# Optimization experiments

Hardware: AMD Instinct MI355X
Metric: run time of the kernel (lower is better)

Reference implementation:

```python
import jax, jax.numpy as jnp
import numpy as np

N = 100000   # nodes
E = 1600000  # directed edges
D_IN, D_HID, D_OUT, N_CLS = 128, 256, 128, 10
EPS = 1e-5


def gcn_conv(x, W, b, src, dst, n):
    # PyG GCNConv: h = XW, add self loops, sym-normalize, scatter-add to dst, + bias
    h = x @ W
    loop = jnp.arange(n)
    src_f = jnp.concatenate([src, loop])
    dst_f = jnp.concatenate([dst, loop])
    deg = jax.ops.segment_sum(jnp.ones(src_f.shape[0], h.dtype), dst_f, num_segments=n)
    dinv = jnp.where(deg > 0, jax.lax.rsqrt(deg), jnp.zeros_like(deg))
    norm = dinv[src_f] * dinv[dst_f]                    # [E+N]
    out = jax.ops.segment_sum(h[src_f] * norm[:, None], dst_f, num_segments=n)
    return out + b


def batchnorm(x, gamma, beta):
    # training-mode BatchNorm1d (batch statistics, biased variance)
    mu = x.mean(0)
    var = x.var(0)
    return gamma * (x - mu) * jax.lax.rsqrt(var + EPS) + beta


def setup_inputs() -> dict:
    key = jax.random.key(0)
    ks = jax.random.split(key, 12)
    x = jax.random.normal(ks[0], (N, D_IN), jnp.float32)
    edge_index = jax.random.randint(ks[1], (2, E), 0, N, dtype=jnp.int64)
    def lin(k, fi, fo):
        s = 1.0 / np.sqrt(fi)
        return jax.random.uniform(k, (fi, fo), jnp.float32, -s, s)
    return {
        "x": x, "edge_index": edge_index,
        "W1": lin(ks[2], D_IN, D_HID), "b1": jnp.zeros(D_HID, jnp.float32),
        "g1": jnp.ones(D_HID, jnp.float32), "beta1": jnp.zeros(D_HID, jnp.float32),
        "W2": lin(ks[3], D_HID, D_HID), "b2": jnp.zeros(D_HID, jnp.float32),
        "g2": jnp.ones(D_HID, jnp.float32), "beta2": jnp.zeros(D_HID, jnp.float32),
        "W3": lin(ks[4], D_HID, D_OUT), "b3": jnp.zeros(D_OUT, jnp.float32),
        "g3": jnp.ones(D_OUT, jnp.float32), "beta3": jnp.zeros(D_OUT, jnp.float32),
        "Wout": lin(ks[5], D_OUT, N_CLS), "bout": jnp.zeros(N_CLS, jnp.float32),
    }


def reference(x, edge_index, W1, b1, g1, beta1, W2, b2, g2, beta2,
              W3, b3, g3, beta3, Wout, bout):
    src, dst = edge_index[0], edge_index[1]
    h = jax.nn.relu(batchnorm(gcn_conv(x, W1, b1, src, dst, N), g1, beta1))
    h = jax.nn.relu(batchnorm(gcn_conv(h, W2, b2, src, dst, N), g2, beta2))
    h = jax.nn.relu(batchnorm(gcn_conv(h, W3, b3, src, dst, N), g3, beta3))
    return h @ Wout + bout
```

## Files before the change

kernel.cpp:

```cpp
#include <hip/hip_runtime.h>
#include <hip/hip_fp16.h>
#include <cstdint>
#include <cstddef>

#define EPS_BN 1e-5f
#define NSLICE 16

static inline int cdiv(int a, int b) { return (a + b - 1) / b; }

using half8   = __attribute__((ext_vector_type(8))) _Float16;
using floatx4 = __attribute__((ext_vector_type(4))) float;

__device__ __forceinline__ float atomAddF(float* p, float v) {
    return unsafeAtomicAdd(p, v);
}


__global__ __launch_bounds__(256) void k_hist(const int* __restrict__ dst, int E,
                                              int NBLK, int NBUCK, int* __restrict__ H) {
    __shared__ int h[256];
    int t = threadIdx.x;
    h[t] = 0;
    __syncthreads();
    int base = blockIdx.x * 4096;
#pragma unroll
    for (int j = 0; j < 16; ++j) {
        int e = base + j * 256 + t;
        if (e < E) atomicAdd(&h[dst[e] >> 9], 1);
    }
    __syncthreads();
    if (t < NBUCK) H[t * NBLK + blockIdx.x] = h[t];
}

__global__ __launch_bounds__(256) void k_scan_reduce(const int* __restrict__ in, int m,
                                                     int* __restrict__ bsum) {
    int base = blockIdx.x * 1024;
    int t = threadIdx.x;
    int s = 0;
#pragma unroll
    for (int i = 0; i < 4; ++i) {
        int idx = base + t * 4 + i;
        if (idx < m) s += in[idx];
    }
    __shared__ int sm[256];
    sm[t] = s;
    __syncthreads();
    for (int off = 128; off > 0; off >>= 1) {
        if (t < off) sm[t] += sm[t + off];
        __syncthreads();
    }
    if (t == 0) bsum[blockIdx.x] = sm[0];
}

__global__ void k_scan_bsum(int* __restrict__ bsum, int nb) {
    if (threadIdx.x == 0 && blockIdx.x == 0) {
        int acc = 0;
        for (int i = 0; i < nb; ++i) { int v = bsum[i]; bsum[i] = acc; acc += v; }
    }
}

__global__ __launch_bounds__(256) void k_scan_final(const int* __restrict__ in, int m,
                                                    const int* __restrict__ bsum,
                                                    int* __restrict__ outS) {
    int base = blockIdx.x * 1024;
    int t = threadIdx.x;
    int v[4];
    int s = 0;
#pragma unroll
    for (int i = 0; i < 4; ++i) {
        int idx = base + t * 4 + i;
        v[i] = (idx < m) ? in[idx] : 0;
        s += v[i];
    }
    __shared__ int sm[256];
    sm[t] = s;
    __syncthreads();
    for (int off = 1; off < 256; off <<= 1) {
        int x = (t >= off) ? sm[t - off] : 0;
        __syncthreads();
        sm[t] += x;
        __syncthreads();
    }
    int excl = sm[t] - s + bsum[blockIdx.x];
#pragma unroll
    for (int i = 0; i < 4; ++i) {
        int idx = base + t * 4 + i;
        if (idx < m) { outS[idx] = excl; excl += v[i]; }
    }
}

__global__ __launch_bounds__(256) void k_bucket(const int* __restrict__ src,
                                                const int* __restrict__ dst, int E,
                                                int NBLK, int NBUCK,
                                                const int* __restrict__ S,
                                                unsigned* __restrict__ pairs) {
    __shared__ int cur[256];
    int t = threadIdx.x;
    if (t < NBUCK) cur[t] = S[t * NBLK + blockIdx.x];
    __syncthreads();
    int base = blockIdx.x * 4096;
#pragma unroll
    for (int j = 0; j < 16; ++j) {
        int e = base + j * 256 + t;
        if (e < E) {
            unsigned s = (unsigned)src[e];
            unsigned d = (unsigned)dst[e];
            int p = atomicAdd(&cur[d >> 9], 1);
            pairs[p] = ((d & 511u) << 17) | s;
        }
    }
}

__global__ __launch_bounds__(256) void k_build(const unsigned* __restrict__ pairs,
                                               const int* __restrict__ S,
                                               int NBLK, int NBUCK, int n, int E,
                                               int* __restrict__ endoff,
                                               float* __restrict__ dinv,
                                               int* __restrict__ csr) {
    int b = blockIdx.x;
    int nbase = b << 9;
    int bstart = S[b * NBLK];
    int bend = (b == NBUCK - 1) ? E : S[(b + 1) * NBLK];
    int t = threadIdx.x;
    __shared__ int sdeg[512];
    __shared__ int scur[512];
    __shared__ int stmp[256];
    sdeg[t] = 0; sdeg[t + 256] = 0;
    __syncthreads();
    for (int e = bstart + t; e < bend; e += 256)
        atomicAdd(&sdeg[pairs[e] >> 17], 1);
    __syncthreads();
    int d0 = sdeg[2 * t], d1 = sdeg[2 * t + 1];
    int ps = d0 + d1;
    stmp[t] = ps;
    __syncthreads();
    for (int off = 1; off < 256; off <<= 1) {
        int x = (t >= off) ? stmp[t - off] : 0;
        __syncthreads();
        stmp[t] += x;
        __syncthreads();
    }
    int c0 = bstart + stmp[t] - ps;
    int c1 = c0 + d0;
    scur[2 * t] = c0;
    scur[2 * t + 1] = c1;
    int v0 = nbase + 2 * t, v1 = v0 + 1;
    if (v0 < n) { endoff[v0] = c1;      dinv[v0] = rsqrtf((float)(d0 + 1)); }
    if (v1 < n) { endoff[v1] = c1 + d1; dinv[v1] = rsqrtf((float)(d1 + 1)); }
    __syncthreads();
    for (int e = bstart + t; e < bend; e += 256) {
        unsigned p = pairs[e];
        int pos = atomicAdd(&scur[p >> 17], 1);
        csr[pos] = (int)(p & 0x1FFFFu);
    }
}

__global__ __launch_bounds__(256) void k_prep(const float* __restrict__ x,
                                              const float* __restrict__ dinv,
                                              const float* __restrict__ W1,
                                              const float* __restrict__ W2,
                                              const float* __restrict__ W3,
                                              __half* __restrict__ xh,
                                              __half* __restrict__ Wt1,
                                              __half* __restrict__ Wt2,
                                              __half* __restrict__ Wt3,
                                              float* __restrict__ stats, int n) {
    int idx = blockIdx.x * 256 + threadIdx.x;
    int nx = n * 16;
    if (idx < nx) {
        int row = idx >> 4;
        float dv = dinv[row];
        const float4* p = (const float4*)x + (size_t)idx * 2;
        float4 a = p[0], b = p[1];
        uint4 o; __half2* oh = (__half2*)&o;
        oh[0] = __floats2half2_rn(a.x * dv, a.y * dv);
        oh[1] = __floats2half2_rn(a.z * dv, a.w * dv);
        oh[2] = __floats2half2_rn(b.x * dv, b.y * dv);
        oh[3] = __floats2half2_rn(b.z * dv, b.w * dv);
        ((uint4*)xh)[idx] = o;
        return;
    }
    int r = idx - nx;
    if (r < 32768) {
        int k = r >> 8, c = r & 255;
        Wt1[c * 128 + k] = __float2half(W1[r]);
    } else if (r < 98304) {
        int r2 = r - 32768;
        int k = r2 >> 8, c = r2 & 255;
        Wt2[c * 256 + k] = __float2half(W2[r2]);
    } else if (r < 131072) {
        int r2 = r - 98304;
        int k = r2 >> 7, c = r2 & 127;
        Wt3[c * 256 + k] = __float2half(W3[r2]);
    } else if (r < 131072 + NSLICE * 256 * 6) {
        stats[r - 131072] = 0.f;
    }
}

__device__ __forceinline__ void acc8(float* acc, uint4 d) {
    const __half2* h = (const __half2*)&d;
#pragma unroll
    for (int j = 0; j < 4; ++j) {
        float2 f = __half22float2(h[j]);
        acc[2 * j] += f.x; acc[2 * j + 1] += f.y;
    }
}

template<int D, bool STATS>
__global__ __launch_bounds__(256, 8) void k_gather_h(const int* __restrict__ csr,
                                                     const int* __restrict__ endoff,
                                                     const __half* __restrict__ P,
                                                     const float* __restrict__ dinv,
                                                     __half* __restrict__ S, int n,
                                                     float* __restrict__ sums,
                                                     float* __restrict__ sqs) {
    constexpr int LPN = D / 8;
    constexpr int NPB = 256 / LPN;
    __shared__ float red[STATS ? 2048 : 1];
    int t = threadIdx.x;
    int lane = t % LPN;
    int sub = t / LPN;
    int v = blockIdx.x * NPB + sub;
    float ov[8];
#pragma unroll
    for (int j = 0; j < 8; ++j) ov[j] = 0.f;
    if (v < n) {
        int beg = (v == 0) ? 0 : endoff[v - 1];
        int end = endoff[v];
        float acc[8];
        {
            uint4 d = *((const uint4*)(P + (size_t)v * D) + lane);
            const __half2* h = (const __half2*)&d;
#pragma unroll
            for (int j = 0; j < 4; ++j) {
                float2 f = __half22float2(h[j]);
                acc[2 * j] = f.x; acc[2 * j + 1] = f.y;
            }
        }
        int i = beg;
        int rem = (end - beg) & 3;
        if (rem & 2) {
            uint4 d0 = *((const uint4*)(P + (size_t)csr[i] * D) + lane);
            uint4 d1 = *((const uint4*)(P + (size_t)csr[i + 1] * D) + lane);
            acc8(acc, d0); acc8(acc, d1);
            i += 2;
        }
        if (rem & 1) {
            uint4 d0 = *((const uint4*)(P + (size_t)csr[i] * D) + lane);
            acc8(acc, d0);
            i += 1;
        }
        if (i < end) {
            uint4 a[4];
#pragma unroll
            for (int u = 0; u < 4; ++u)
                a[u] = *((const uint4*)(P + (size_t)csr[i + u] * D) + lane);
            for (i += 4; i < end; i += 4) {
                uint4 b[4];
#pragma unroll
                for (int u = 0; u < 4; ++u)
                    b[u] = *((const uint4*)(P + (size_t)csr[i + u] * D) + lane);
#pragma unroll
                for (int u = 0; u < 4; ++u) acc8(acc, a[u]);
#pragma unroll
                for (int u = 0; u < 4; ++u) a[u] = b[u];
            }
#pragma unroll
            for (int u = 0; u < 4; ++u) acc8(acc, a[u]);
        }
        float dv = dinv[v];
        uint4 o; __half2* oh = (__half2*)&o;
#pragma unroll
        for (int j = 0; j < 4; ++j) {
            float a0 = acc[2 * j] * dv, a1 = acc[2 * j + 1] * dv;
            oh[j] = __floats2half2_rn(a0, a1);
            ov[2 * j] = a0; ov[2 * j + 1] = a1;
        }
        *((uint4*)(S + (size_t)v * D) + lane) = o;
    }
    if (STATS) {
        int slice = blockIdx.x & (NSLICE - 1);
#pragma unroll
        for (int j = 0; j < 8; ++j) red[t * 8 + j] = ov[j];
        __syncthreads();
        if (t < D) {
            int lc = t >> 3, j = t & 7;
            float ts = 0.f;
#pragma unroll
            for (int s = 0; s < NPB; ++s) ts += red[(s * LPN + lc) * 8 + j];
            atomAddF(&sums[slice * 256 + t], ts);
        }
        __syncthreads();
#pragma unroll
        for (int j = 0; j < 8; ++j) red[t * 8 + j] = ov[j] * ov[j];
        __syncthreads();
        if (t < D) {
            int lc = t >> 3, j = t & 7;
            float tq = 0.f;
#pragma unroll
            for (int s = 0; s < NPB; ++s) tq += red[(s * LPN + lc) * 8 + j];
            atomAddF(&sqs[slice * 256 + t], tq);
        }
    }
}

template<int K, int NC, bool SCALE, bool BNIN, bool STATS>
__global__ __launch_bounds__(256) void k_gemm_mfma(const __half* __restrict__ A,
                                                   const __half* __restrict__ Wt,
                                                   const float* __restrict__ dinv,
                                                   const float* __restrict__ isum,
                                                   const float* __restrict__ isq,
                                                   const float* __restrict__ g,
                                                   const float* __restrict__ beta,
                                                   float* __restrict__ osum,
                                                   float* __restrict__ osq,
                                                   __half* __restrict__ C, int n) {
    constexpr int LDA = 40;
    __shared__ _Float16 As[128 * LDA];
    __shared__ _Float16 Bs[128 * LDA];
    __shared__ float ssc[BNIN ? K : 1];
    __shared__ float ssh[BNIN ? K : 1];
    __shared__ float scs[STATS ? 128 : 1];
    __shared__ float scq[STATS ? 128 : 1];
    int tid = threadIdx.x;
    if (BNIN) {
        float nf = (float)n;
        for (int i = tid; i < K; i += 256) {
            float su = 0.f, sq = 0.f;
#pragma unroll
            for (int s = 0; s < NSLICE; ++s) {
                su += isum[s * 256 + i];
                sq += isq[s * 256 + i];
            }
            float mu = su / nf;
            float var = sq / nf - mu * mu;
            float sc = g[i] * rsqrtf(var + EPS_BN);
            ssc[i] = sc; ssh[i] = beta[i] - mu * sc;
        }
        __syncthreads();
    }
    int wave = tid >> 6, lane = tid & 63;
    int wr = wave >> 1, wc = wave & 1;
    int q = lane >> 4, l16 = lane & 15;
    int row0 = blockIdx.x * 128;
    int col0 = blockIdx.y * 128;
    floatx4 acc[4][4];
#pragma unroll
    for (int r = 0; r < 4; ++r)
#pragma unroll
        for (int c = 0; c < 4; ++c) acc[r][c] = (floatx4)0.0f;

    for (int k0 = 0; k0 < K; k0 += 32) {
#pragma unroll
        for (int i = 0; i < 2; ++i) {
            int s = tid + i * 256;
            int r = s >> 2, ks = s & 3;
            uint4 d = *(const uint4*)(A + (size_t)(row0 + r) * K + k0 + ks * 8);
            if (BNIN) {
                const __half2* h = (const __half2*)&d;
                uint4 o; __half2* oh = (__half2*)&o;
                int kb = k0 + ks * 8;
#pragma unroll
                for (int j = 0; j < 4; ++j) {
                    float2 f = __half22float2(h[j]);
                    float y0 = fmaxf(0.f, f.x * ssc[kb + 2 * j]     + ssh[kb + 2 * j]);
                    float y1 = fmaxf(0.f, f.y * ssc[kb + 2 * j + 1] + ssh[kb + 2 * j + 1]);
                    oh[j] = __floats2half2_rn(y0, y1);
                }
                d = o;
            }
            *(uint4*)&As[r * LDA + ks * 8] = d;
        }
#pragma unroll
        for (int i = 0; i < 2; ++i) {
            int s = tid + i * 256;
            int r = s >> 2, ks = s & 3;
            uint4 d = *(const uint4*)(Wt + (size_t)(col0 + r) * K + k0 + ks * 8);
            *(uint4*)&Bs[r * LDA + ks * 8] = d;
        }
        __syncthreads();
        half8 af[4], bf[4];
#pragma unroll
        for (int r = 0; r < 4; ++r)
            af[r] = *(const half8*)&As[(wr * 64 + r * 16 + l16) * LDA + q * 8];
#pragma unroll
        for (int c = 0; c < 4; ++c)
            bf[c] = *(const half8*)&Bs[(wc * 64 + c * 16 + l16) * LDA + q * 8];
#pragma unroll
        for (int r = 0; r < 4; ++r)
#pragma unroll
            for (int c = 0; c < 4; ++c)
                acc[r][c] = __builtin_amdgcn_mfma_f32_16x16x32_f16(af[r], bf[c], acc[r][c], 0, 0, 0);
        __syncthreads();
    }
    float colsum[4] = {};
    float colsq[4]  = {};
#pragma unroll
    for (int r = 0; r < 4; ++r) {
#pragma unroll
        for (int reg = 0; reg < 4; ++reg) {
            int grow = row0 + wr * 64 + r * 16 + q * 4 + reg;
            float sc = 1.f;
            if (SCALE) sc = (grow < n) ? dinv[grow] : 0.f;
            __half* cp = C + (size_t)grow * NC + col0 + wc * 64 + l16;
#pragma unroll
            for (int c = 0; c < 4; ++c) {
                float v = acc[r][c][reg] * sc;
                cp[c * 16] = __float2half(v);
                if (STATS && grow < n) { colsum[c] += v; colsq[c] += v * v; }
            }
        }
    }
    if (STATS) {
        if (tid < 128) { scs[tid] = 0.f; scq[tid] = 0.f; }
        __syncthreads();
#pragma unroll
        for (int c = 0; c < 4; ++c) {
            atomicAdd(&scs[wc * 64 + c * 16 + l16], colsum[c]);
            atomicAdd(&scq[wc * 64 + c * 16 + l16], colsq[c]);
        }
        __syncthreads();
        if (tid < 128) {
            int slice = blockIdx.x & (NSLICE - 1);
            atomAddF(&osum[slice * 256 + col0 + tid], scs[tid]);
            atomAddF(&osq[slice * 256 + col0 + tid], scq[tid]);
        }
    }
}

__global__ __launch_bounds__(256) void k_out(const __half* __restrict__ H,
                                             const float* __restrict__ sums,
                                             const float* __restrict__ sqs,
                                             const float* __restrict__ g,
                                             const float* __restrict__ beta,
                                             const float* __restrict__ Wout,
                                             const float* __restrict__ bout,
                                             float* __restrict__ out, int n) {
    __shared__ float Wl[128 * 10];
    __shared__ float bl[10];
    __shared__ float osc[128];
    __shared__ float osh[128];
    __shared__ float red[256 * 10];
    int tid = threadIdx.x;
    for (int i = tid; i < 1280; i += 256) Wl[i] = Wout[i];
    if (tid < 10) bl[tid] = bout[tid];
    if (tid < 128) {
        float nf = (float)n;
        float su = 0.f, sq = 0.f;
#pragma unroll
        for (int s = 0; s < NSLICE; ++s) {
            su += sums[s * 256 + tid];
            sq += sqs[s * 256 + tid];
        }
        float mu = su / nf;
        float var = sq / nf - mu * mu;
        float sc = g[tid] * rsqrtf(var + EPS_BN);
        osc[tid] = sc; osh[tid] = beta[tid] - mu * sc;
    }
    __syncthreads();
    int rl = tid >> 1;
    int h2 = tid & 1;
    int r = blockIdx.x * 128 + rl;
    float p[10] = {};
    if (r < n) {
        const __half* a = H + (size_t)r * 128 + h2 * 64;
#pragma unroll 8
        for (int k = 0; k < 64; ++k) {
            int col = h2 * 64 + k;
            float av = fmaxf(0.f, __half2float(a[k]) * osc[col] + osh[col]);
            const float* wr = Wl + col * 10;
#pragma unroll
            for (int c = 0; c < 10; ++c) p[c] += av * wr[c];
        }
    }
    float* rr = red + (size_t)tid * 10;
#pragma unroll
    for (int c = 0; c < 10; ++c) rr[c] = p[c];
    __syncthreads();
    if (h2 == 0 && r < n) {
        const float* rb = red + (size_t)tid * 10;
#pragma unroll
        for (int c = 0; c < 10; ++c) {
            out[(size_t)r * 10 + c] = rb[c] + rb[10 + c] + bl[c];
        }
    }
}

extern "C" void kernel_launch(void* const* d_in, const int* in_sizes, int n_in,
                              void* d_out, int out_size, void* d_ws, size_t ws_size,
                              hipStream_t stream) {
    const float* x    = (const float*)d_in[0];
    const int*   ei   = (const int*)d_in[1];
    const float* W1   = (const float*)d_in[2];
    const float* g1   = (const float*)d_in[4];
    const float* be1  = (const float*)d_in[5];
    const float* W2   = (const float*)d_in[6];
    const float* g2   = (const float*)d_in[8];
    const float* be2  = (const float*)d_in[9];
    const float* W3   = (const float*)d_in[10];
    const float* g3   = (const float*)d_in[12];
    const float* be3  = (const float*)d_in[13];
    const float* Wout = (const float*)d_in[14];
    const float* bout = (const float*)d_in[15];
    float* out = (float*)d_out;

    int n = in_sizes[0] / 128;
    int E = in_sizes[1] / 2;
    const int* esrc = ei;
    const int* edst = ei + E;
    int npad = cdiv(n, 128) * 128;
    int NBLK = cdiv(E, 4096);
    int NBUCK = (n + 511) >> 9;
    if (NBUCK > 256) return;
    int m = NBUCK * NBLK;
    int nb2 = cdiv(m, 1024);

    const size_t align = 256;
    auto al = [&](size_t s) { return (s + align - 1) & ~(align - 1); };
    size_t n4 = al((size_t)n * 4 + 512);

    const size_t statsLayer = (size_t)NSLICE * 256 * 2 * 4;
    const size_t statsTotal = statsLayer * 3;

    char* ws = (char*)d_ws;
    size_t o_end   = 0;
    size_t o_dinv  = o_end + n4;
    size_t o_stats = o_dinv + n4;
    size_t o_bsum  = o_stats + statsTotal;
    size_t o_H     = o_bsum + 1024;
    size_t o_Hs    = o_H + al((size_t)m * 4);
    size_t o_csr   = o_Hs + al((size_t)m * 4);
    size_t o_pairs = o_csr + al((size_t)E * 4);
    size_t o_w1    = o_pairs + al((size_t)E * 4);
    size_t o_w2    = o_w1 + al(256 * 128 * 2);
    size_t o_w3    = o_w2 + al(256 * 256 * 2);
    size_t o_A128a = o_w3 + al(128 * 256 * 2);
    size_t o_A128b = o_A128a + al((size_t)npad * 128 * 2);
    size_t o_A256a = o_A128b + al((size_t)npad * 128 * 2);
    size_t o_A256b = o_A256a + al((size_t)npad * 256 * 2);
    size_t need    = o_A256b + (size_t)npad * 256 * 2;
    if (ws_size < need) return;

    int*      endoff = (int*)(ws + o_end);
    float*    dinv   = (float*)(ws + o_dinv);
    float*    stats  = (float*)(ws + o_stats);
    float*    sums1  = stats;
    float*    sqs1   = sums1 + NSLICE * 256;
    float*    sums2  = (float*)(ws + o_stats + statsLayer);
    float*    sqs2   = sums2 + NSLICE * 256;
    float*    sums3  = (float*)(ws + o_stats + 2 * statsLayer);
    float*    sqs3   = sums3 + NSLICE * 256;
    int*      bsum   = (int*)(ws + o_bsum);
    int*      H      = (int*)(ws + o_H);
    int*      Hs     = (int*)(ws + o_Hs);
    int*      csr    = (int*)(ws + o_csr);
    unsigned* pairs  = (unsigned*)(ws + o_pairs);
    __half*   Wt1    = (__half*)(ws + o_w1);
    __half*   Wt2    = (__half*)(ws + o_w2);
    __half*   Wt3    = (__half*)(ws + o_w3);
    __half*   xh     = (__half*)(ws + o_A128a);
    __half*   S3     = (__half*)(ws + o_A128a);
    __half*   G1     = (__half*)(ws + o_A128b);
    __half*   P3     = (__half*)(ws + o_A128b);
    __half*   P1     = (__half*)(ws + o_A256a);
    __half*   S2     = (__half*)(ws + o_A256a);
    __half*   P2     = (__half*)(ws + o_A256b);

    k_hist<<<NBLK, 256, 0, stream>>>(edst, E, NBLK, NBUCK, H);
    k_scan_reduce<<<nb2, 256, 0, stream>>>(H, m, bsum);
    k_scan_bsum<<<1, 64, 0, stream>>>(bsum, nb2);
    k_scan_final<<<nb2, 256, 0, stream>>>(H, m, bsum, Hs);
    k_bucket<<<NBLK, 256, 0, stream>>>(esrc, edst, E, NBLK, NBUCK, Hs, pairs);
    k_build<<<NBUCK, 256, 0, stream>>>(pairs, Hs, NBLK, NBUCK, n, E, endoff, dinv, csr);

    int prepTotal = n * 16 + 131072 + NSLICE * 256 * 6;
    k_prep<<<cdiv(prepTotal, 256), 256, 0, stream>>>(
        x, dinv, W1, W2, W3, xh, Wt1, Wt2, Wt3, stats, n);

    k_gather_h<128, false><<<cdiv(n, 16), 256, 0, stream>>>(
        csr, endoff, xh, dinv, G1, n, nullptr, nullptr);
    k_gemm_mfma<128, 256, false, false, true><<<dim3(npad / 128, 2), 256, 0, stream>>>(
        G1, Wt1, dinv, nullptr, nullptr, nullptr, nullptr, sums1, sqs1, P1, n);

    k_gemm_mfma<256, 256, true, true, false><<<dim3(npad / 128, 2), 256, 0, stream>>>(
        P1, Wt2, dinv, sums1, sqs1, g1, be1, nullptr, nullptr, P2, n);
    k_gather_h<256, true><<<cdiv(n, 8), 256, 0, stream>>>(
        csr, endoff, P2, dinv, S2, n, sums2, sqs2);

    k_gemm_mfma<256, 128, true, true, false><<<dim3(npad / 128, 1), 256, 0, stream>>>(
        S2, Wt3, dinv, sums2, sqs2, g2, be2, nullptr, nullptr, P3, n);
    k_gather_h<128, true><<<cdiv(n, 16), 256, 0, stream>>>(
        csr, endoff, P3, dinv, S3, n, sums3, sqs3);

    k_out<<<cdiv(n, 128), 256, 0, stream>>>(S3, sums3, sqs3, g3, be3, Wout, bout, out, n);
}
```

Before: 568.0 us.

## Split gather into 64-column slices and sort CSR neighbors by source chunk

The CSR build now sub-buckets each destination's neighbor list into 8 chunks by source-ID range and stores per-chunk end offsets. The gather kernel is restructured so each block handles one 64-column feature slice for 32 nodes, with block IDs interleaved so concurrently running blocks touch the same source range and column slice. The aim is to improve L2/MALL locality for the random neighbor-row reads. In exchange it uses 8x larger offset arrays, reads more offsets per node, and adds loop overhead for small chunks, and the inner unrolling is reduced from 4 loads in flight to 2.

```diff
diff --git a/kernel.cpp b/kernel.cpp
--- a/kernel.cpp
+++ b/kernel.cpp
@@ -5,6 +5,7 @@
 
 #define EPS_BN 1e-5f
 #define NSLICE 16
+#define NCHUNK 8
 
 static inline int cdiv(int a, int b) { return (a + b - 1) / b; }
 
@@ -113,7 +114,7 @@
 
 __global__ __launch_bounds__(256) void k_build(const unsigned* __restrict__ pairs,
                                                const int* __restrict__ S,
-                                               int NBLK, int NBUCK, int n, int E,
+                                               int NBLK, int NBUCK, int n, int E, int sh,
                                                int* __restrict__ endoff,
                                                float* __restrict__ dinv,
                                                int* __restrict__ csr) {
@@ -122,17 +123,23 @@
     int bstart = S[b * NBLK];
     int bend = (b == NBUCK - 1) ? E : S[(b + 1) * NBLK];
     int t = threadIdx.x;
-    __shared__ int sdeg[512];
-    __shared__ int scur[512];
+    __shared__ int sdeg[4096];
+    __shared__ int scur[4096];
     __shared__ int stmp[256];
-    sdeg[t] = 0; sdeg[t + 256] = 0;
-    __syncthreads();
-    for (int e = bstart + t; e < bend; e += 256)
-        atomicAdd(&sdeg[pairs[e] >> 17], 1);
-    __syncthreads();
-    int d0 = sdeg[2 * t], d1 = sdeg[2 * t + 1];
-    int ps = d0 + d1;
-    stmp[t] = ps;
+#pragma unroll
+    for (int i = 0; i < 16; ++i) sdeg[t + i * 256] = 0;
+    __syncthreads();
+    for (int e = bstart + t; e < bend; e += 256) {
+        unsigned p = pairs[e];
+        int key = (int)((p >> 17) << 3) | (int)((p & 0x1FFFFu) >> sh);
+        atomicAdd(&sdeg[key], 1);
+    }
+    __syncthreads();
+    int loc[16];
+    int ls = 0;
+#pragma unroll
+    for (int i = 0; i < 16; ++i) { loc[i] = sdeg[t * 16 + i]; ls += loc[i]; }
+    stmp[t] = ls;
     __syncthreads();
     for (int off = 1; off < 256; off <<= 1) {
         int x = (t >= off) ? stmp[t - off] : 0;
@@ -140,17 +147,25 @@
         stmp[t] += x;
         __syncthreads();
     }
-    int c0 = bstart + stmp[t] - ps;
-    int c1 = c0 + d0;
-    scur[2 * t] = c0;
-    scur[2 * t + 1] = c1;
+    int run = bstart + stmp[t] - ls;
+    int d0 = 0, d1 = 0;
     int v0 = nbase + 2 * t, v1 = v0 + 1;
-    if (v0 < n) { endoff[v0] = c1;      dinv[v0] = rsqrtf((float)(d0 + 1)); }
-    if (v1 < n) { endoff[v1] = c1 + d1; dinv[v1] = rsqrtf((float)(d1 + 1)); }
+#pragma unroll
+    for (int i = 0; i < 16; ++i) {
+        scur[t * 16 + i] = run;
+        int e_ = run + loc[i];
+        int v = (i < 8) ? v0 : v1;
+        if (v < n) endoff[(size_t)v * NCHUNK + (i & 7)] = e_;
+        run = e_;
+        if (i < 8) d0 += loc[i]; else d1 += loc[i];
+    }
+    if (v0 < n) dinv[v0] = rsqrtf((float)(d0 + 1));
+    if (v1 < n) dinv[v1] = rsqrtf((float)(d1 + 1));
     __syncthreads();
     for (int e = bstart + t; e < bend; e += 256) {
         unsigned p = pairs[e];
-        int pos = atomicAdd(&scur[p >> 17], 1);
+        int key = (int)((p >> 17) << 3) | (int)((p & 0x1FFFFu) >> sh);
+        int pos = atomicAdd(&scur[key], 1);
         csr[pos] = (int)(p & 0x1FFFFu);
     }
 }
@@ -207,29 +222,34 @@
 }
 
 template<int D, bool STATS>
-__global__ __launch_bounds__(256, 8) void k_gather_h(const int* __restrict__ csr,
-                                                     const int* __restrict__ endoff,
-                                                     const __half* __restrict__ P,
-                                                     const float* __restrict__ dinv,
-                                                     __half* __restrict__ S, int n,
-                                                     float* __restrict__ sums,
-                                                     float* __restrict__ sqs) {
-    constexpr int LPN = D / 8;
-    constexpr int NPB = 256 / LPN;
+__global__ __launch_bounds__(256, 8) void k_gather2(const int* __restrict__ csr,
+                                                    const int* __restrict__ endoff,
+                                                    const __half* __restrict__ P,
+                                                    const float* __restrict__ dinv,
+                                                    __half* __restrict__ S, int n,
+                                                    float* __restrict__ sums,
+                                                    float* __restrict__ sqs) {
+    constexpr int NSL = D / 64;
     __shared__ float red[STATS ? 2048 : 1];
+    int bid = blockIdx.x;
+    int x8 = bid & 7;
+    int slice, gidx;
+    if (NSL == 4) { slice = x8 >> 1; gidx = (bid >> 3) * 2 + (x8 & 1); }
+    else          { slice = x8 >> 2; gidx = (bid >> 3) * 4 + (x8 & 3); }
+    int Gn = (n + 31) >> 5;
+    if (gidx >= Gn) return;
     int t = threadIdx.x;
-    int lane = t % LPN;
-    int sub = t / LPN;
-    int v = blockIdx.x * NPB + sub;
+    int lane = t & 7;
+    int sub = t >> 3;
+    int v = gidx * 32 + sub;
+    const __half* Pb = P + (size_t)slice * 64 + lane * 8;
     float ov[8];
 #pragma unroll
     for (int j = 0; j < 8; ++j) ov[j] = 0.f;
     if (v < n) {
-        int beg = (v == 0) ? 0 : endoff[v - 1];
-        int end = endoff[v];
         float acc[8];
         {
-            uint4 d = *((const uint4*)(P + (size_t)v * D) + lane);
+            uint4 d = *(const uint4*)(Pb + (size_t)v * D);
             const __half2* h = (const __half2*)&d;
 #pragma unroll
             for (int j = 0; j < 4; ++j) {
@@ -237,36 +257,23 @@
                 acc[2 * j] = f.x; acc[2 * j + 1] = f.y;
             }
         }
-        int i = beg;
-        int rem = (end - beg) & 3;
-        if (rem & 2) {
-            uint4 d0 = *((const uint4*)(P + (size_t)csr[i] * D) + lane);
-            uint4 d1 = *((const uint4*)(P + (size_t)csr[i + 1] * D) + lane);
-            acc8(acc, d0); acc8(acc, d1);
-            i += 2;
-        }
-        if (rem & 1) {
-            uint4 d0 = *((const uint4*)(P + (size_t)csr[i] * D) + lane);
-            acc8(acc, d0);
-            i += 1;
-        }
-        if (i < end) {
-            uint4 a[4];
-#pragma unroll
-            for (int u = 0; u < 4; ++u)
-                a[u] = *((const uint4*)(P + (size_t)csr[i + u] * D) + lane);
-            for (i += 4; i < end; i += 4) {
-                uint4 b[4];
-#pragma unroll
-                for (int u = 0; u < 4; ++u)
-                    b[u] = *((const uint4*)(P + (size_t)csr[i + u] * D) + lane);
-#pragma unroll
-                for (int u = 0; u < 4; ++u) acc8(acc, a[u]);
-#pragma unroll
-                for (int u = 0; u < 4; ++u) a[u] = b[u];
+        size_t idx0 = (size_t)v * NCHUNK;
+        int beg = (idx0 == 0) ? 0 : endoff[idx0 - 1];
+#pragma unroll 1
+        for (int c = 0; c < NCHUNK; ++c) {
+            int end = endoff[idx0 + c];
+            int i = beg;
+            if ((end - i) & 1) {
+                uint4 d0 = *(const uint4*)(Pb + (size_t)csr[i] * D);
+                acc8(acc, d0);
+                ++i;
             }
-#pragma unroll
-            for (int u = 0; u < 4; ++u) acc8(acc, a[u]);
+            for (; i < end; i += 2) {
+                uint4 d0 = *(const uint4*)(Pb + (size_t)csr[i] * D);
+                uint4 d1 = *(const uint4*)(Pb + (size_t)csr[i + 1] * D);
+                acc8(acc, d0); acc8(acc, d1);
+            }
+            beg = end;
         }
         float dv = dinv[v];
         uint4 o; __half2* oh = (__half2*)&o;
@@ -276,30 +283,30 @@
             oh[j] = __floats2half2_rn(a0, a1);
             ov[2 * j] = a0; ov[2 * j + 1] = a1;
         }
-        *((uint4*)(S + (size_t)v * D) + lane) = o;
+        *(uint4*)(S + (size_t)v * D + slice * 64 + lane * 8) = o;
     }
     if (STATS) {
-        int slice = blockIdx.x & (NSLICE - 1);
+        int shard = bid & (NSLICE - 1);
 #pragma unroll
         for (int j = 0; j < 8; ++j) red[t * 8 + j] = ov[j];
         __syncthreads();
-        if (t < D) {
-            int lc = t >> 3, j = t & 7;
+        if (t < 64) {
+            int ln = t >> 3, j = t & 7;
             float ts = 0.f;
 #pragma unroll
-            for (int s = 0; s < NPB; ++s) ts += red[(s * LPN + lc) * 8 + j];
-            atomAddF(&sums[slice * 256 + t], ts);
+            for (int s = 0; s < 32; ++s) ts += red[(s * 8 + ln) * 8 + j];
+            atomAddF(&sums[shard * 256 + slice * 64 + t], ts);
         }
         __syncthreads();
 #pragma unroll
         for (int j = 0; j < 8; ++j) red[t * 8 + j] = ov[j] * ov[j];
         __syncthreads();
-        if (t < D) {
-            int lc = t >> 3, j = t & 7;
+        if (t < 64) {
+            int ln = t >> 3, j = t & 7;
             float tq = 0.f;
 #pragma unroll
-            for (int s = 0; s < NPB; ++s) tq += red[(s * LPN + lc) * 8 + j];
-            atomAddF(&sqs[slice * 256 + t], tq);
+            for (int s = 0; s < 32; ++s) tq += red[(s * 8 + ln) * 8 + j];
+            atomAddF(&sqs[shard * 256 + slice * 64 + t], tq);
         }
     }
 }
@@ -514,17 +521,20 @@
     if (NBUCK > 256) return;
     int m = NBUCK * NBLK;
     int nb2 = cdiv(m, 1024);
+    int sh = 0;
+    while ((NCHUNK << sh) < n) ++sh;
 
     const size_t align = 256;
     auto al = [&](size_t s) { return (s + align - 1) & ~(align - 1); };
-    size_t n4 = al((size_t)n * 4 + 512);
+    size_t n4  = al((size_t)n * 4 + 512);
+    size_t nE8 = al((size_t)n * NCHUNK * 4 + 512);
 
     const size_t statsLayer = (size_t)NSLICE * 256 * 2 * 4;
     const size_t statsTotal = statsLayer * 3;
 
     char* ws = (char*)d_ws;
     size_t o_end   = 0;
-    size_t o_dinv  = o_end + n4;
+    size_t o_dinv  = o_end + nE8;
     size_t o_stats = o_dinv + n4;
     size_t o_bsum  = o_stats + statsTotal;
     size_t o_H     = o_bsum + 1024;
@@ -571,25 +581,29 @@
     k_scan_bsum<<<1, 64, 0, stream>>>(bsum, nb2);
     k_scan_final<<<nb2, 256, 0, stream>>>(H, m, bsum, Hs);
     k_bucket<<<NBLK, 256, 0, stream>>>(esrc, edst, E, NBLK, NBUCK, Hs, pairs);
-    k_build<<<NBUCK, 256, 0, stream>>>(pairs, Hs, NBLK, NBUCK, n, E, endoff, dinv, csr);
+    k_build<<<NBUCK, 256, 0, stream>>>(pairs, Hs, NBLK, NBUCK, n, E, sh, endoff, dinv, csr);
 
     int prepTotal = n * 16 + 131072 + NSLICE * 256 * 6;
     k_prep<<<cdiv(prepTotal, 256), 256, 0, stream>>>(
         x, dinv, W1, W2, W3, xh, Wt1, Wt2, Wt3, stats, n);
 
-    k_gather_h<128, false><<<cdiv(n, 16), 256, 0, stream>>>(
+    int Gn = (n + 31) >> 5;
+    int grid128 = 8 * cdiv(Gn, 4);
+    int grid256 = 8 * cdiv(Gn, 2);
+
+    k_gather2<128, false><<<grid128, 256, 0, stream>>>(
         csr, endoff, xh, dinv, G1, n, nullptr, nullptr);
     k_gemm_mfma<128, 256, false, false, true><<<dim3(npad / 128, 2), 256, 0, stream>>>(
         G1, Wt1, dinv, nullptr, nullptr, nullptr, nullptr, sums1, sqs1, P1, n);
 
     k_gemm_mfma<256, 256, true, true, false><<<dim3(npad / 128, 2), 256, 0, stream>>>(
         P1, Wt2, dinv, sums1, sqs1, g1, be1, nullptr, nullptr, P2, n);
-    k_gather_h<256, true><<<cdiv(n, 8), 256, 0, stream>>>(
+    k_gather2<256, true><<<grid256, 256, 0, stream>>>(
         csr, endoff, P2, dinv, S2, n, sums2, sqs2);
 
     k_gemm_mfma<256, 128, true, true, false><<<dim3(npad / 128, 1), 256, 0, stream>>>(
         S2, Wt3, dinv, sums2, sqs2, g2, be2, nullptr, nullptr, P3, n);
-    k_gather_h<128, true><<<cdiv(n, 16), 256, 0, stream>>>(
+    k_gather2<128, true><<<grid128, 256, 0, stream>>>(
         csr, endoff, P3, dinv, S3, n, sums3, sqs3);
 
     k_out<<<cdiv(n, 128), 256, 0, stream>>>(S3, sums3, sqs3, g3, be3, Wout, bout, out, n);
```

Result: slower. 632.4 us (+11.3%).
